# Performance work log

Hardware: AMD Instinct MI355X
Metric: run time of the kernel (lower is better)

Reference implementation:

```python
import jax, jax.numpy as jnp
import numpy as np
import math

B, T, NC = 16, 256, 2
_NS = (9, 9, 11, 11, 9, 20)  # legacy6 region node counts
_OUT, _RF, _FD, _NH, _FF = 32, 64, 128, 4, 2048


def _region_adj(n):
    # chain + second-order edges (legacy6), plus self-loops; GCN sym-normalized
    A = np.zeros((n, n), np.float32)
    for i in range(n - 1):
        A[i, i + 1] = A[i + 1, i] = 1.0
    for i in range(n - 2):
        A[i, i + 2] = A[i + 2, i] = 1.0
    A = A + np.eye(n, dtype=np.float32)
    d = A.sum(1) ** -0.5
    return jnp.asarray(d[:, None] * A * d[None, :])

_ADJS = [_region_adj(n) for n in _NS]


def _pe_table(t, d):
    pos = np.arange(t, dtype=np.float32)[:, None]
    div = np.exp(np.arange(0, d, 2, dtype=np.float32) * (-math.log(10000.0) / d))
    pe = np.zeros((t, d), np.float32)
    pe[:, 0::2] = np.sin(pos * div)
    pe[:, 1::2] = np.cos(pos * div)
    return jnp.asarray(pe)

_PE = _pe_table(T, _FD)


def _ln(x, g, b, eps=1e-5):
    m = jnp.mean(x, -1, keepdims=True)
    v = jnp.mean((x - m) ** 2, -1, keepdims=True)
    return (x - m) / jnp.sqrt(v + eps) * g + b


def _mha(q, kv, qkv_w, qkv_b, ow, ob, nh):
    d = q.shape[-1]
    hd = d // nh
    wq, wk, wv = jnp.split(qkv_w, 3, axis=1)
    bq, bk, bv = jnp.split(qkv_b, 3)
    def sp(x):
        return x.reshape(x.shape[0], x.shape[1], nh, hd).transpose(0, 2, 1, 3)
    Q, K, V = sp(q @ wq + bq), sp(kv @ wk + bk), sp(kv @ wv + bv)
    att = jax.nn.softmax(jnp.einsum('bhqd,bhkd->bhqk', Q, K) / jnp.sqrt(jnp.float32(hd)), axis=-1)
    o = jnp.einsum('bhqk,bhkd->bhqd', att, V).transpose(0, 2, 1, 3).reshape(q.shape[0], q.shape[1], d)
    return o @ ow + ob


def _tel(x, qkv_w, qkv_b, ow, ob, l1g, l1b, f1w, f1b, f2w, f2b, l2g, l2b, nh):
    # torch post-norm TransformerEncoderLayer (relu FFN, eval mode: no dropout)
    x = _ln(x + _mha(x, x, qkv_w, qkv_b, ow, ob, nh), l1g, l1b)
    ff = jax.nn.relu(x @ f1w + f1b) @ f2w + f2b
    return _ln(x + ff, l2g, l2b)


def setup_inputs() -> dict:
    key = jax.random.key(0)
    ks = iter(jax.random.split(key, 80))
    def nrm(shape, s=0.05):
        return jax.random.normal(next(ks), shape, jnp.float32) * s
    inp = {}
    for name, n in zip(('x_ljaw', 'x_rjaw', 'x_leye', 'x_reye', 'x_nose', 'x_mouth'), _NS):
        inp[name] = jax.random.normal(next(ks), (B, T, n, 11), jnp.float32)
    inp['global_feats'] = jax.random.normal(next(ks), (B, T, 4), jnp.float32)
    inp['global_alpha'] = jnp.float32(0.2)
    inp['gcn1_w'] = nrm((6, 11, _OUT)); inp['gcn1_b'] = jnp.zeros((6, _OUT))
    inp['gcn2_w'] = nrm((6, _OUT, _OUT)); inp['gcn2_b'] = jnp.zeros((6, _OUT))
    inp['rln_g'] = jnp.ones((6, _RF)); inp['rln_b'] = jnp.zeros((6, _RF))
    inp['sp_qkv_w'] = nrm((_RF, 3 * _RF)); inp['sp_qkv_b'] = jnp.zeros((3 * _RF,))
    inp['sp_out_w'] = nrm((_RF, _RF)); inp['sp_out_b'] = jnp.zeros((_RF,))
    inp['sp_ln1_g'] = jnp.ones((_RF,)); inp['sp_ln1_b'] = jnp.zeros((_RF,))
    inp['sp_ff1_w'] = nrm((_RF, _FF)); inp['sp_ff1_b'] = jnp.zeros((_FF,))
    inp['sp_ff2_w'] = nrm((_FF, _RF)); inp['sp_ff2_b'] = jnp.zeros((_RF,))
    inp['sp_ln2_g'] = jnp.ones((_RF,)); inp['sp_ln2_b'] = jnp.zeros((_RF,))
    priors = np.array([0.3, 0.3, 0.8, 0.8, 0.4, 1.0], np.float32)
    inp['region_logits'] = jnp.asarray(np.log(np.expm1(priors)).reshape(1, 6, 1))
    inp['gate1_w'] = nrm((_RF, 32)); inp['gate1_b'] = jnp.zeros((32,))
    inp['gate2_w'] = nrm((32, 1)); inp['gate2_b'] = jnp.zeros((1,))
    inp['ca_qkv_w'] = nrm((_RF, 3 * _RF)); inp['ca_qkv_b'] = jnp.zeros((3 * _RF,))
    inp['ca_out_w'] = nrm((_RF, _RF)); inp['ca_out_b'] = jnp.zeros((_RF,))
    inp['ca_ln_g'] = jnp.ones((_RF,)); inp['ca_ln_b'] = jnp.zeros((_RF,))
    inp['glob_w'] = nrm((4, _RF)); inp['glob_b'] = jnp.zeros((_RF,))
    inp['glob_ln_g'] = jnp.ones((_RF,)); inp['glob_ln_b'] = jnp.zeros((_RF,))
    inp['fused_ln_g'] = jnp.ones((_FD,)); inp['fused_ln_b'] = jnp.zeros((_FD,))
    inp['tp_qkv_w'] = nrm((_FD, 3 * _FD)); inp['tp_qkv_b'] = jnp.zeros((3 * _FD,))
    inp['tp_out_w'] = nrm((_FD, _FD)); inp['tp_out_b'] = jnp.zeros((_FD,))
    inp['tp_ln1_g'] = jnp.ones((_FD,)); inp['tp_ln1_b'] = jnp.zeros((_FD,))
    inp['tp_ff1_w'] = nrm((_FD, _FF)); inp['tp_ff1_b'] = jnp.zeros((_FF,))
    inp['tp_ff2_w'] = nrm((_FF, _FD)); inp['tp_ff2_b'] = jnp.zeros((_FD,))
    inp['tp_ln2_g'] = jnp.ones((_FD,)); inp['tp_ln2_b'] = jnp.zeros((_FD,))
    inp['attnproj_w'] = nrm((_FD, 1)); inp['attnproj_b'] = jnp.zeros((1,))
    inp['cls1_w'] = nrm((_FD, _OUT)); inp['cls1_b'] = jnp.zeros((_OUT,))
    inp['cls_ln_g'] = jnp.ones((_OUT,)); inp['cls_ln_b'] = jnp.zeros((_OUT,))
    inp['cls2_w'] = nrm((_OUT, NC)); inp['cls2_b'] = jnp.zeros((NC,))
    return inp


def reference(x_ljaw, x_rjaw, x_leye, x_reye, x_nose, x_mouth, global_feats, global_alpha, gcn1_w, gcn1_b, gcn2_w, gcn2_b, rln_g, rln_b, sp_qkv_w, sp_qkv_b, sp_out_w, sp_out_b, sp_ln1_g, sp_ln1_b, sp_ff1_w, sp_ff1_b, sp_ff2_w, sp_ff2_b, sp_ln2_g, sp_ln2_b, region_logits, gate1_w, gate1_b, gate2_w, gate2_b, ca_qkv_w, ca_qkv_b, ca_out_w, ca_out_b, ca_ln_g, ca_ln_b, glob_w, glob_b, glob_ln_g, glob_ln_b, fused_ln_g, fused_ln_b, tp_qkv_w, tp_qkv_b, tp_out_w, tp_out_b, tp_ln1_g, tp_ln1_b, tp_ff1_w, tp_ff1_b, tp_ff2_w, tp_ff2_b, tp_ln2_g, tp_ln2_b, attnproj_w, attnproj_b, cls1_w, cls1_b, cls_ln_g, cls_ln_b, cls2_w, cls2_b):
    xs = (x_ljaw, x_rjaw, x_leye, x_reye, x_nose, x_mouth)
    Bc, Tc = x_ljaw.shape[0], x_ljaw.shape[1]
    # per-region 2-layer GCN + concat(mean,max) node pooling -> (B,T,64) tokens
    toks = []
    for i in range(6):
        A = _ADJS[i]
        h = jax.nn.relu(jnp.einsum('nm,btmf->btnf', A, xs[i] @ gcn1_w[i]) + gcn1_b[i])
        h = jax.nn.relu(jnp.einsum('nm,btmf->btnf', A, h @ gcn2_w[i]) + gcn2_b[i])
        feat = jnp.concatenate([h.mean(2), h.max(2)], -1)
        toks.append(_ln(feat, rln_g[i], rln_b[i]))
    tok = jnp.stack(toks, 2).reshape(Bc * Tc, 6, _RF)
    # spatial transformer over the 6 region tokens per frame
    tok = _tel(tok, sp_qkv_w, sp_qkv_b, sp_out_w, sp_out_b, sp_ln1_g, sp_ln1_b, sp_ff1_w, sp_ff1_b, sp_ff2_w, sp_ff2_b, sp_ln2_g, sp_ln2_b, _NH)
    # learned region priors (softplus) * per-sample sigmoid gates
    rw = jax.nn.softplus(region_logits)
    gate = jax.nn.sigmoid(jax.nn.relu(tok @ gate1_w + gate1_b) @ gate2_w + gate2_b)
    tok = tok * rw * gate
    # cross-attn fusion: mean-region query attends over region tokens
    q = jnp.mean(tok, 1, keepdims=True)
    attn = _mha(q, tok, ca_qkv_w, ca_qkv_b, ca_out_w, ca_out_b, _NH)
    fused_r = _ln(q[:, 0] + attn[:, 0], ca_ln_g, ca_ln_b)
    # gated global branch (4 -> 64), concat to fused_dim=128
    g = jax.nn.relu(_ln(global_feats.reshape(Bc * Tc, 4) @ glob_w + glob_b, glob_ln_g, glob_ln_b))
    g = jnp.tanh(global_alpha) * g
    fused = _ln(jnp.concatenate([fused_r, g], -1), fused_ln_g, fused_ln_b).reshape(Bc, Tc, _FD)
    # temporal transformer + attention pooling over time
    fused = fused + _PE[None, :Tc]
    h = _tel(fused, tp_qkv_w, tp_qkv_b, tp_out_w, tp_out_b, tp_ln1_g, tp_ln1_b, tp_ff1_w, tp_ff1_b, tp_ff2_w, tp_ff2_b, tp_ln2_g, tp_ln2_b, _NH)
    wt = jax.nn.softmax(h @ attnproj_w + attnproj_b, axis=1)
    pooled = jnp.sum(wt * h, 1)
    z = jax.nn.relu(_ln(pooled @ cls1_w + cls1_b, cls_ln_g, cls_ln_b))
    return z @ cls2_w + cls2_b
```

## Files before the change

kernel.cpp:

```cpp
#include <hip/hip_runtime.h>
#include <math.h>
#include <stddef.h>

#define NFRM 4096
#define NBATCH 16

typedef __attribute__((ext_vector_type(8))) short short8v;
typedef __attribute__((ext_vector_type(4))) float f32x4;
#define MFMA_BF16(a,b,c) __builtin_amdgcn_mfma_f32_16x16x32_bf16(a,b,c,0,0,0)

__device__ inline float wsum64(float v){
  #pragma unroll
  for(int m=32;m>=1;m>>=1) v += __shfl_xor(v, m, 64);
  return v;
}

__device__ inline float pe_val(int t,int d){
  int k = d >> 1;
  float div = expf(-(float)(2*k) * (9.210340371976184f/128.f));
  float ang = (float)t * div;
  return (d & 1) ? cosf(ang) : sinf(ang);
}

__device__ inline void bf16split(float x, unsigned short &h, unsigned short &l){
  unsigned u = __float_as_uint(x);
  unsigned r = (u + 0x7FFFu + ((u>>16)&1u)) & 0xFFFF0000u;
  h = (unsigned short)(r>>16);
  float rem = x - __uint_as_float(r);
  unsigned u2 = __float_as_uint(rem);
  unsigned r2 = (u2 + 0x7FFFu + ((u2>>16)&1u));
  l = (unsigned short)(r2>>16);
}

__global__ __launch_bounds__(64) void pack_all_kernel(
    const float* __restrict__ spf1w, const float* __restrict__ spf2w,
    const float* __restrict__ tpf1w, const float* __restrict__ tpf2w,
    unsigned short* __restrict__ sp1h, unsigned short* __restrict__ sp1l,
    unsigned short* __restrict__ sp2h, unsigned short* __restrict__ sp2l,
    unsigned short* __restrict__ tp1h, unsigned short* __restrict__ tp1l,
    unsigned short* __restrict__ tp2h, unsigned short* __restrict__ tp2l)
{
  int b = blockIdx.x, lane = threadIdx.x;
  const float* w; unsigned short *hi, *lo; int K, N, ntile, s;
  if(b < 256){        w=spf1w; hi=sp1h; lo=sp1l; K=64;   N=2048; ntile=b&127;        s=b>>7; }
  else if(b < 512){   int bb=b-256;  w=spf2w; hi=sp2h; lo=sp2l; K=2048; N=64;   ntile=bb&3;   s=bb>>2; }
  else if(b < 1024){  int bb=b-512;  w=tpf1w; hi=tp1h; lo=tp1l; K=128;  N=2048; ntile=bb&127; s=bb>>7; }
  else {              int bb=b-1024; w=tpf2w; hi=tp2h; lo=tp2l; K=2048; N=128;  ntile=bb&7;   s=bb>>3; }
  int n = ntile*16 + (lane & 15);
  int k0 = s*32 + (lane>>4)*8;
  size_t off = (((size_t)ntile*(K/32) + s)*64 + lane)*8;
  #pragma unroll
  for(int e=0;e<8;e++){
    float v = w[(size_t)(k0+e)*N + n];
    unsigned short h,l;
    bf16split(v,h,l);
    hi[off+e]=h; lo[off+e]=l;
  }
}

template<int D, int NS>
__global__ __launch_bounds__(256) void ffn_mfma_partial(
    const float* __restrict__ X, float* __restrict__ P,
    const unsigned short* __restrict__ w1h, const unsigned short* __restrict__ w1l,
    const float* __restrict__ b1,
    const unsigned short* __restrict__ w2h, const unsigned short* __restrict__ w2l)
{
  constexpr int TM=32, JC=128;
  constexpr int KS1 = D/32;
  constexpr int NT2W = (D/16)/4;
  constexpr int HS = 2048/NS;
  constexpr int NCH = HS/JC;
  constexpr int HP = JC + 8;
  __shared__ unsigned short Hh[TM][HP];
  __shared__ unsigned short Hl[TM][HP];
  int tid = threadIdx.x;
  int lane = tid & 63, w = tid >> 6;
  int ar = lane & 15, ak = lane >> 4;
  size_t Ntok = (size_t)gridDim.x*TM;
  const float* Xb = X + (size_t)blockIdx.x*TM*D;

  short8v xah[2][KS1], xal[2][KS1];
  #pragma unroll
  for(int mt=0;mt<2;mt++){
    #pragma unroll
    for(int s=0;s<KS1;s++){
      const float* xp = Xb + (size_t)(mt*16+ar)*D + s*32 + ak*8;
      #pragma unroll
      for(int e=0;e<8;e++){
        unsigned short h,l;
        bf16split(xp[e],h,l);
        xah[mt][s][e]=(short)h; xal[mt][s][e]=(short)l;
      }
    }
  }

  f32x4 acc2[2][NT2W];
  #pragma unroll
  for(int mt=0;mt<2;mt++)
    #pragma unroll
    for(int nt=0;nt<NT2W;nt++)
      acc2[mt][nt] = (f32x4){0.f,0.f,0.f,0.f};

  for(int ch=0; ch<NCH; ch++){
    int jc = blockIdx.y*HS + ch*JC;
    f32x4 a1[2][2];
    #pragma unroll
    for(int mt=0;mt<2;mt++){ a1[mt][0]=(f32x4){0,0,0,0}; a1[mt][1]=(f32x4){0,0,0,0}; }
    #pragma unroll
    for(int s=0;s<KS1;s++){
      #pragma unroll
      for(int nt=0;nt<2;nt++){
        int ntile1 = (jc + w*32 + nt*16) >> 4;
        size_t off = (((size_t)ntile1*KS1 + s)*64 + lane)*8;
        short8v bh = *(const short8v*)(w1h + off);
        short8v bl = *(const short8v*)(w1l + off);
        #pragma unroll
        for(int mt=0;mt<2;mt++){
          a1[mt][nt] = MFMA_BF16(xah[mt][s], bh, a1[mt][nt]);
          a1[mt][nt] = MFMA_BF16(xah[mt][s], bl, a1[mt][nt]);
          a1[mt][nt] = MFMA_BF16(xal[mt][s], bh, a1[mt][nt]);
        }
      }
    }
    __syncthreads();
    #pragma unroll
    for(int nt=0;nt<2;nt++){
      int colBase = w*32 + nt*16 + ar;
      float bval = b1[jc + colBase];
      #pragma unroll
      for(int mt=0;mt<2;mt++){
        #pragma unroll
        for(int r=0;r<4;r++){
          float hv = a1[mt][nt][r] + bval;
          hv = fmaxf(hv, 0.f);
          unsigned short h,l;
          bf16split(hv,h,l);
          int row = mt*16 + ak*4 + r;
          Hh[row][colBase]=h; Hl[row][colBase]=l;
        }
      }
    }
    __syncthreads();
    #pragma unroll
    for(int s2=0;s2<4;s2++){
      short8v ah[2], al[2];
      #pragma unroll
      for(int mt=0;mt<2;mt++){
        ah[mt] = *(const short8v*)&Hh[mt*16+ar][s2*32 + ak*8];
        al[mt] = *(const short8v*)&Hl[mt*16+ar][s2*32 + ak*8];
      }
      #pragma unroll
      for(int nt=0;nt<NT2W;nt++){
        int ntile2 = w*NT2W + nt;
        int kstep2 = (jc >> 5) + s2;
        size_t off = (((size_t)ntile2*64 + kstep2)*64 + lane)*8;
        short8v bh = *(const short8v*)(w2h + off);
        short8v bl = *(const short8v*)(w2l + off);
        #pragma unroll
        for(int mt=0;mt<2;mt++){
          acc2[mt][nt] = MFMA_BF16(ah[mt], bh, acc2[mt][nt]);
          acc2[mt][nt] = MFMA_BF16(ah[mt], bl, acc2[mt][nt]);
          acc2[mt][nt] = MFMA_BF16(al[mt], bh, acc2[mt][nt]);
        }
      }
    }
  }
  float* Pb = P + (size_t)blockIdx.y*Ntok*D + (size_t)blockIdx.x*TM*D;
  #pragma unroll
  for(int mt=0;mt<2;mt++){
    #pragma unroll
    for(int nt=0;nt<NT2W;nt++){
      int col = (w*NT2W + nt)*16 + ar;
      #pragma unroll
      for(int r=0;r<4;r++){
        int row = mt*16 + ak*4 + r;
        Pb[(size_t)row*D + col] = acc2[mt][nt][r];
      }
    }
  }
}

template<int D, int NS>
__global__ __launch_bounds__(256) void ffn_combine_kernel(
    const float* __restrict__ X, const float* __restrict__ P,
    float* __restrict__ Y,
    const float* __restrict__ b2,
    const float* __restrict__ lg, const float* __restrict__ lb)
{
  constexpr int EPL = D/64;
  int tid=threadIdx.x;
  int lane = tid & 63;
  size_t Ntok = (size_t)gridDim.x*4;
  size_t row = (size_t)blockIdx.x*4 + (tid>>6);
  size_t base = row*D;
  float e[EPL];
  float s=0.f;
  #pragma unroll
  for(int i=0;i<EPL;i++){
    int c = i*64+lane;
    float v = X[base+c] + b2[c];
    #pragma unroll
    for(int sp=0;sp<NS;sp++) v += P[(size_t)sp*Ntok*D + base + c];
    e[i]=v; s+=v;
  }
  float mm = wsum64(s)*(1.f/D);
  float s2=0.f;
  #pragma unroll
  for(int i=0;i<EPL;i++){ float d=e[i]-mm; s2+=d*d; }
  float rs = rsqrtf(wsum64(s2)*(1.f/D)+1e-5f);
  #pragma unroll
  for(int i=0;i<EPL;i++){
    int c=i*64+lane;
    Y[base+c] = (e[i]-mm)*rs*lg[c]+lb[c];
  }
}

__global__ __launch_bounds__(128) void gcn_kernel(
    const float* __restrict__ x0,const float* __restrict__ x1,
    const float* __restrict__ x2,const float* __restrict__ x3,
    const float* __restrict__ x4,const float* __restrict__ x5,
    const float* __restrict__ g1w,const float* __restrict__ g1b,
    const float* __restrict__ g2w,const float* __restrict__ g2b,
    const float* __restrict__ rg,const float* __restrict__ rb,
    float* __restrict__ tok)
{
  int tid=threadIdx.x;
  int lane = tid & 63, w = tid >> 6;
  int f = blockIdx.x*2 + w;
  int r = blockIdx.y;
  int n = (r==5) ? 20 : ((r==2 || r==3) ? 11 : 9);
  const float* xr = (r==0)?x0:(r==1)?x1:(r==2)?x2:(r==3)?x3:(r==4)?x4:x5;
  int c = lane & 31;

  __shared__ float xs[2][20*12];
  __shared__ float t0g[2][24*32];
  __shared__ float t1s[2][20*32];
  __shared__ float Cw[2][20][5];

  float W1c[11], W2c[32];
  #pragma unroll
  for(int k=0;k<11;k++) W1c[k]=g1w[r*352 + k*32 + c];
  #pragma unroll
  for(int k=0;k<32;k++) W2c[k]=g2w[r*1024 + k*32 + c];
  float b1c = g1b[r*32+c], b2c = g2b[r*32+c];

  for(int i=lane;i<100;i+=64){
    int node=i/5, j=i%5, m=node+j-2;
    float cf=0.f;
    if(node<n && m>=0 && m<n){
      int di = 1 + min(node,2) + min(n-1-node,2);
      int dm = 1 + min(m,2) + min(n-1-m,2);
      cf = rsqrtf((float)(di*dm));
    }
    Cw[w][node][j]=cf;
  }
  for(int i=lane;i<128;i+=64){
    int row4=i>>5, col=i&31;
    int row = (row4<2) ? row4 : (n+row4);
    t0g[w][row*32+col]=0.f;
  }
  for(int i=lane;i<n*12;i+=64){
    int node=i/12, k=i-node*12;
    xs[w][i] = (k<11) ? xr[(size_t)f*n*11 + node*11 + k] : 0.f;
  }
  __builtin_amdgcn_wave_barrier();
  for(int i=lane;i<n*32;i+=64){
    int node=i>>5;
    float4 xa = *(const float4*)&xs[w][node*12];
    float4 xb = *(const float4*)&xs[w][node*12+4];
    float4 xc = *(const float4*)&xs[w][node*12+8];
    float s = xa.x*W1c[0]+xa.y*W1c[1]+xa.z*W1c[2]+xa.w*W1c[3]
            + xb.x*W1c[4]+xb.y*W1c[5]+xb.z*W1c[6]+xb.w*W1c[7]
            + xc.x*W1c[8]+xc.y*W1c[9]+xc.z*W1c[10];
    t0g[w][(node+2)*32+c]=s;
  }
  __builtin_amdgcn_wave_barrier();
  for(int i=lane;i<n*32;i+=64){
    int node=i>>5;
    float s=b1c;
    #pragma unroll
    for(int j=0;j<5;j++) s += Cw[w][node][j]*t0g[w][(node+j)*32+c];
    t1s[w][i]=fmaxf(s,0.f);
  }
  __builtin_amdgcn_wave_barrier();
  for(int i=lane;i<n*32;i+=64){
    int node=i>>5;
    float s=0.f;
    #pragma unroll
    for(int k0=0;k0<32;k0+=4){
      float4 tv = *(const float4*)&t1s[w][node*32+k0];
      s += tv.x*W2c[k0] + tv.y*W2c[k0+1] + tv.z*W2c[k0+2] + tv.w*W2c[k0+3];
    }
    t0g[w][(node+2)*32+c]=s;
  }
  __builtin_amdgcn_wave_barrier();
  for(int i=lane;i<n*32;i+=64){
    int node=i>>5;
    float s=b2c;
    #pragma unroll
    for(int j=0;j<5;j++) s += Cw[w][node][j]*t0g[w][(node+j)*32+c];
    t1s[w][i]=fmaxf(s,0.f);
  }
  __builtin_amdgcn_wave_barrier();
  float v;
  if(lane<32){
    float s=0.f;
    for(int m=0;m<n;m++) s += t1s[w][m*32+lane];
    v = s/(float)n;
  } else {
    float mx=-1e30f;
    for(int m=0;m<n;m++) mx = fmaxf(mx, t1s[w][m*32+c]);
    v = mx;
  }
  float m1 = wsum64(v)*(1.f/64.f);
  float d1 = v - m1;
  float var = wsum64(d1*d1)*(1.f/64.f);
  float y = d1*rsqrtf(var+1e-5f)*rg[r*64+lane] + rb[r*64+lane];
  tok[((size_t)f*6+r)*64+lane] = y;
}

__global__ __launch_bounds__(256) void sp_attn_kernel(
    float* __restrict__ tok,
    const float* __restrict__ qkvw,const float* __restrict__ qkvb,
    const float* __restrict__ ow,const float* __restrict__ ob,
    const float* __restrict__ l1g,const float* __restrict__ l1b)
{
  __shared__ float Xs[24][64];
  __shared__ float QKV[24][192];
  __shared__ float SC[4][144];
  __shared__ float AO[24][64];
  int tid=threadIdx.x;
  int f0 = blockIdx.x*4;
  float* Xf = &Xs[0][0];
  for(int i=tid;i<1536;i+=256) Xf[i] = tok[(size_t)f0*384 + i];
  __syncthreads();
  {
    int cg = tid & 31, c0 = cg*6;
    int rg = tid >> 5, r0 = rg*3;
    float acc[3][6];
    #pragma unroll
    for(int m=0;m<3;m++)
      #pragma unroll
      for(int j=0;j<6;j++) acc[m][j]=qkvb[c0+j];
    for(int k=0;k<64;k++){
      float wv[6];
      #pragma unroll
      for(int j=0;j<6;j++) wv[j]=qkvw[k*192+c0+j];
      float xv0=Xs[r0][k], xv1=Xs[r0+1][k], xv2=Xs[r0+2][k];
      #pragma unroll
      for(int j=0;j<6;j++){
        acc[0][j]+=xv0*wv[j];
        acc[1][j]+=xv1*wv[j];
        acc[2][j]+=xv2*wv[j];
      }
    }
    #pragma unroll
    for(int m=0;m<3;m++)
      #pragma unroll
      for(int j=0;j<6;j++) QKV[r0+m][c0+j]=acc[m][j];
  }
  __syncthreads();
  for(int i=tid;i<576;i+=256){
    int fr=i/144, rest=i%144;
    int h=rest/36, qi=(rest%36)/6, ki=rest%6;
    float s=0.f;
    #pragma unroll
    for(int d=0;d<16;d++) s += QKV[fr*6+qi][h*16+d]*QKV[fr*6+ki][64+h*16+d];
    SC[fr][rest]=s*0.25f;
  }
  __syncthreads();
  if(tid<96){
    int fr=tid/24, idx=tid%24;
    int base=idx*6;
    float mx=-1e30f;
    for(int k=0;k<6;k++) mx=fmaxf(mx,SC[fr][base+k]);
    float sm=0.f;
    for(int k=0;k<6;k++){ float e=expf(SC[fr][base+k]-mx); SC[fr][base+k]=e; sm+=e; }
    float rr=1.f/sm;
    for(int k=0;k<6;k++) SC[fr][base+k]*=rr;
  }
  __syncthreads();
  for(int i=tid;i<1536;i+=256){
    int fr=i/384, rem=i%384;
    int row=rem/64, c=rem&63, h=c/16;
    float s=0.f;
    #pragma unroll
    for(int k=0;k<6;k++) s += SC[fr][h*36+row*6+k]*QKV[fr*6+k][128+c];
    AO[fr*6+row][c]=s;
  }
  __syncthreads();
  {
    int cg = tid & 31, c0 = cg*2;
    int rg = tid >> 5, r0 = rg*3;
    float acc[3][2];
    #pragma unroll
    for(int m=0;m<3;m++){ acc[m][0]=ob[c0]; acc[m][1]=ob[c0+1]; }
    for(int k=0;k<64;k++){
      float w0=ow[k*64+c0], w1=ow[k*64+c0+1];
      float a0=AO[r0][k], a1=AO[r0+1][k], a2=AO[r0+2][k];
      acc[0][0]+=a0*w0; acc[0][1]+=a0*w1;
      acc[1][0]+=a1*w0; acc[1][1]+=a1*w1;
      acc[2][0]+=a2*w0; acc[2][1]+=a2*w1;
    }
    #pragma unroll
    for(int m=0;m<3;m++){
      QKV[r0+m][c0]   = Xs[r0+m][c0]   + acc[m][0];
      QKV[r0+m][c0+1] = Xs[r0+m][c0+1] + acc[m][1];
    }
  }
  __syncthreads();
  {
    int lane = tid & 63, w = tid >> 6;
    #pragma unroll
    for(int rr=0;rr<6;rr++){
      int row = w*6+rr;
      float v=QKV[row][lane];
      float mm=wsum64(v)*(1.f/64.f);
      float d=v-mm;
      float var=wsum64(d*d)*(1.f/64.f);
      tok[(size_t)f0*384 + row*64 + lane]=d*rsqrtf(var+1e-5f)*l1g[lane]+l1b[lane];
    }
  }
}

template<int D, int TM>
__global__ __launch_bounds__(256) void ffn_ln_kernel(
    const float* __restrict__ X, float* __restrict__ Yout,
    const float* __restrict__ w1,const float* __restrict__ b1,
    const float* __restrict__ w2,const float* __restrict__ b2,
    const float* __restrict__ lg,const float* __restrict__ lb)
{
  constexpr int JC = 128;
  constexpr int JS = JC + 4;
  constexpr int M1 = TM/8;
  constexpr int CG = D/4;
  constexpr int MG2 = 256/CG;
  constexpr int M2 = TM/MG2;
  __shared__ float Xs[TM*D];
  __shared__ float Hs[TM*JS];
  int tid=threadIdx.x;
  const float* Xb = X + (size_t)blockIdx.x*TM*D;
  for(int i=tid;i<TM*D;i+=256) Xs[i]=Xb[i];

  int jg = tid & 31, j0 = jg*4;
  int mg1 = tid >> 5;
  int m10 = mg1*M1;
  int cg = tid % CG, c0 = cg*4;
  int mg2 = tid / CG;
  int m20 = mg2*M2;

  float acc[M2][4];
  #pragma unroll
  for(int m=0;m<M2;m++){ acc[m][0]=0.f;acc[m][1]=0.f;acc[m][2]=0.f;acc[m][3]=0.f; }

  __syncthreads();
  for(int jc=0;jc<2048;jc+=JC){
    float a1[M1][4];
    float4 bv = *(const float4*)&b1[jc+j0];
    #pragma unroll
    for(int m=0;m<M1;m++){ a1[m][0]=bv.x;a1[m][1]=bv.y;a1[m][2]=bv.z;a1[m][3]=bv.w; }
    for(int k0=0;k0<D;k0+=4){
      float4 wr0 = *(const float4*)&w1[(size_t)(k0+0)*2048 + jc + j0];
      float4 wr1 = *(const float4*)&w1[(size_t)(k0+1)*2048 + jc + j0];
      float4 wr2 = *(const float4*)&w1[(size_t)(k0+2)*2048 + jc + j0];
      float4 wr3 = *(const float4*)&w1[(size_t)(k0+3)*2048 + jc + j0];
      #pragma unroll
      for(int m=0;m<M1;m++){
        float4 xv = *(const float4*)&Xs[(m10+m)*D + k0];
        a1[m][0] += xv.x*wr0.x + xv.y*wr1.x + xv.z*wr2.x + xv.w*wr3.x;
        a1[m][1] += xv.x*wr0.y + xv.y*wr1.y + xv.z*wr2.y + xv.w*wr3.y;
        a1[m][2] += xv.x*wr0.z + xv.y*wr1.z + xv.z*wr2.z + xv.w*wr3.z;
        a1[m][3] += xv.x*wr0.w + xv.y*wr1.w + xv.z*wr2.w + xv.w*wr3.w;
      }
    }
    #pragma unroll
    for(int m=0;m<M1;m++){
      float4 hv;
      hv.x=fmaxf(a1[m][0],0.f); hv.y=fmaxf(a1[m][1],0.f);
      hv.z=fmaxf(a1[m][2],0.f); hv.w=fmaxf(a1[m][3],0.f);
      *(float4*)&Hs[(m10+m)*JS + j0] = hv;
    }
    __syncthreads();
    for(int jj0=0;jj0<JC;jj0+=4){
      float4 w20 = *(const float4*)&w2[(size_t)(jc+jj0+0)*D + c0];
      float4 w21 = *(const float4*)&w2[(size_t)(jc+jj0+1)*D + c0];
      float4 w22 = *(const float4*)&w2[(size_t)(jc+jj0+2)*D + c0];
      float4 w23 = *(const float4*)&w2[(size_t)(jc+jj0+3)*D + c0];
      #pragma unroll
      for(int m=0;m<M2;m++){
        float4 hv = *(const float4*)&Hs[(m20+m)*JS + jj0];
        acc[m][0] += hv.x*w20.x + hv.y*w21.x + hv.z*w22.x + hv.w*w23.x;
        acc[m][1] += hv.x*w20.y + hv.y*w21.y + hv.z*w22.y + hv.w*w23.y;
        acc[m][2] += hv.x*w20.z + hv.y*w21.z + hv.z*w22.z + hv.w*w23.z;
        acc[m][3] += hv.x*w20.w + hv.y*w21.w + hv.z*w22.w + hv.w*w23.w;
      }
    }
    __syncthreads();
  }
  {
    float4 b2v = *(const float4*)&b2[c0];
    #pragma unroll
    for(int m=0;m<M2;m++){
      int row = m20+m;
      float4 xv = *(const float4*)&Xs[row*D + c0];
      float4 yv;
      yv.x = xv.x + acc[m][0] + b2v.x;
      yv.y = xv.y + acc[m][1] + b2v.y;
      yv.z = xv.z + acc[m][2] + b2v.z;
      yv.w = xv.w + acc[m][3] + b2v.w;
      *(float4*)&Hs[row*D + c0] = yv;
    }
  }
  __syncthreads();
  constexpr int EPL = D/64;
  int lane = tid & 63, wv = tid >> 6;
  float* Yb = Yout + (size_t)blockIdx.x*TM*D;
  for(int row=wv; row<TM; row+=4){
    float e[EPL];
    float s=0.f;
    #pragma unroll
    for(int i=0;i<EPL;i++){ e[i]=Hs[row*D + i*64 + lane]; s+=e[i]; }
    float mm = wsum64(s)*(1.f/D);
    float s2=0.f;
    #pragma unroll
    for(int i=0;i<EPL;i++){ float d=e[i]-mm; s2+=d*d; }
    float rs = rsqrtf(wsum64(s2)*(1.f/D)+1e-5f);
    #pragma unroll
    for(int i=0;i<EPL;i++)
      Yb[row*D + i*64 + lane] = (e[i]-mm)*rs*lg[i*64+lane]+lb[i*64+lane];
  }
}

__global__ __launch_bounds__(256) void fuse_kernel(
    const float* __restrict__ tok, const float* __restrict__ gfeat,
    const float* __restrict__ alpha_p, const float* __restrict__ rlogit,
    const float* __restrict__ g1w,const float* __restrict__ g1b,
    const float* __restrict__ g2w,const float* __restrict__ g2b,
    const float* __restrict__ caqw,const float* __restrict__ caqb,
    const float* __restrict__ caow,const float* __restrict__ caob,
    const float* __restrict__ calng,const float* __restrict__ calnb,
    const float* __restrict__ gw,const float* __restrict__ gb,
    const float* __restrict__ glng,const float* __restrict__ glnb,
    const float* __restrict__ flng,const float* __restrict__ flnb,
    float* __restrict__ fused)
{
  int tid=threadIdx.x;
  int lane = tid & 63, w = tid >> 6;
  int f = blockIdx.x*4 + w;
  __shared__ float X[4][384];
  __shared__ float G1[4][192];
  __shared__ float gt[4][6];
  __shared__ float qv[4][64];
  __shared__ float Qs[4][64];
  __shared__ float KK[4][384], VV[4][384];
  __shared__ float sc[4][24];
  __shared__ float AOs[4][64];

  const float* trow = tok + (size_t)f*384;
  for(int i=lane;i<384;i+=64) X[w][i]=trow[i];
  __syncthreads();
  for(int i=lane;i<192;i+=64){
    int rr=i/32, j=i%32;
    float s=g1b[j];
    #pragma unroll
    for(int k=0;k<64;k++) s += X[w][rr*64+k]*g1w[k*32+j];
    G1[w][i]=fmaxf(s,0.f);
  }
  __syncthreads();
  if(lane<6){
    float s=g2b[0];
    #pragma unroll
    for(int k=0;k<32;k++) s += G1[w][lane*32+k]*g2w[k];
    float gate = 1.f/(1.f+expf(-s));
    float rw = log1pf(expf(rlogit[lane]));
    gt[w][lane]=gate*rw;
  }
  __syncthreads();
  for(int i=lane;i<384;i+=64) X[w][i]*=gt[w][i/64];
  __syncthreads();
  {
    float s=0.f;
    #pragma unroll
    for(int rr=0;rr<6;rr++) s+=X[w][rr*64+lane];
    qv[w][lane]=s*(1.f/6.f);
  }
  __syncthreads();
  {
    float s=caqb[lane];
    #pragma unroll
    for(int k=0;k<64;k++) s += qv[w][k]*caqw[k*192+lane];
    Qs[w][lane]=s;
  }
  for(int i=lane;i<384;i+=64){
    int rr=i/64, c=i%64;
    float sk=caqb[64+c], sv=caqb[128+c];
    #pragma unroll
    for(int k=0;k<64;k++){
      float xv=X[w][rr*64+k];
      sk += xv*caqw[k*192+64+c];
      sv += xv*caqw[k*192+128+c];
    }
    KK[w][i]=sk; VV[w][i]=sv;
  }
  __syncthreads();
  if(lane<24){
    int h=lane/6, ki=lane%6;
    float s=0.f;
    #pragma unroll
    for(int d=0;d<16;d++) s += Qs[w][h*16+d]*KK[w][ki*64+h*16+d];
    sc[w][lane]=s*0.25f;
  }
  __syncthreads();
  if(lane<4){
    float mx=-1e30f;
    for(int k=0;k<6;k++) mx=fmaxf(mx,sc[w][lane*6+k]);
    float sm=0.f;
    for(int k=0;k<6;k++){ float e=expf(sc[w][lane*6+k]-mx); sc[w][lane*6+k]=e; sm+=e; }
    float rr=1.f/sm;
    for(int k=0;k<6;k++) sc[w][lane*6+k]*=rr;
  }
  __syncthreads();
  {
    int h=lane/16;
    float s=0.f;
    #pragma unroll
    for(int k=0;k<6;k++) s += sc[w][h*6+k]*VV[w][k*64+lane];
    AOs[w][lane]=s;
  }
  __syncthreads();
  float pr;
  {
    float s=caob[lane];
    #pragma unroll
    for(int k=0;k<64;k++) s += AOs[w][k]*caow[k*64+lane];
    pr = qv[w][lane] + s;
  }
  float m1=wsum64(pr)*(1.f/64.f);
  float d1=pr-m1;
  float v1=wsum64(d1*d1)*(1.f/64.f);
  float fr = d1*rsqrtf(v1+1e-5f)*calng[lane]+calnb[lane];
  float gvv;
  {
    float s=gb[lane];
    #pragma unroll
    for(int k=0;k<4;k++) s += gfeat[(size_t)f*4+k]*gw[k*64+lane];
    gvv=s;
  }
  float m2=wsum64(gvv)*(1.f/64.f);
  float d2=gvv-m2;
  float v2=wsum64(d2*d2)*(1.f/64.f);
  float gg = fmaxf(d2*rsqrtf(v2+1e-5f)*glng[lane]+glnb[lane],0.f)*tanhf(alpha_p[0]);
  float sm_ = wsum64(fr+gg)*(1.f/128.f);
  float da=fr-sm_, db=gg-sm_;
  float vv = wsum64(da*da+db*db)*(1.f/128.f);
  float rs = rsqrtf(vv+1e-5f);
  int t = f & 255;
  fused[(size_t)f*128+lane]     = da*rs*flng[lane]+flnb[lane]         + pe_val(t,lane);
  fused[(size_t)f*128+64+lane]  = db*rs*flng[64+lane]+flnb[64+lane]   + pe_val(t,64+lane);
}

__global__ __launch_bounds__(256) void tqkv_gemm_kernel(
    const float* __restrict__ X, float* __restrict__ Y,
    const float* __restrict__ w, const float* __restrict__ b)
{
  __shared__ float Xs[32*128];
  int tid=threadIdx.x;
  const float* Xb = X + (size_t)blockIdx.x*32*128;
  for(int i=tid;i<4096;i+=256) Xs[i]=Xb[i];
  __syncthreads();
  int cg = tid & 31, c0 = cg*4;
  int mg = tid >> 5, m0 = mg*4;
  float* Yb = Y + (size_t)blockIdx.x*32*384;
  int oc = blockIdx.y*128;
  float acc[4][4];
  float4 bv = *(const float4*)&b[oc+c0];
  #pragma unroll
  for(int m=0;m<4;m++){ acc[m][0]=bv.x;acc[m][1]=bv.y;acc[m][2]=bv.z;acc[m][3]=bv.w; }
  for(int k0=0;k0<128;k0+=4){
    float4 w0 = *(const float4*)&w[(k0+0)*384 + oc + c0];
    float4 w1 = *(const float4*)&w[(k0+1)*384 + oc + c0];
    float4 w2 = *(const float4*)&w[(k0+2)*384 + oc + c0];
    float4 w3 = *(const float4*)&w[(k0+3)*384 + oc + c0];
    #pragma unroll
    for(int m=0;m<4;m++){
      float4 xv = *(const float4*)&Xs[(m0+m)*128 + k0];
      acc[m][0] += xv.x*w0.x + xv.y*w1.x + xv.z*w2.x + xv.w*w3.x;
      acc[m][1] += xv.x*w0.y + xv.y*w1.y + xv.z*w2.y + xv.w*w3.y;
      acc[m][2] += xv.x*w0.z + xv.y*w1.z + xv.z*w2.z + xv.w*w3.z;
      acc[m][3] += xv.x*w0.w + xv.y*w1.w + xv.z*w2.w + xv.w*w3.w;
    }
  }
  #pragma unroll
  for(int m=0;m<4;m++){
    float4 yv; yv.x=acc[m][0];yv.y=acc[m][1];yv.z=acc[m][2];yv.w=acc[m][3];
    *(float4*)&Yb[(m0+m)*384 + oc + c0] = yv;
  }
}

__global__ __launch_bounds__(256) void tattn_split_kernel(
    const float* __restrict__ qkv, float* __restrict__ PO,
    float* __restrict__ PM, float* __restrict__ PL)
{
  int b=blockIdx.x, h=blockIdx.y, s=blockIdx.z, tid=threadIdx.x;
  __shared__ float Ksh[32*32];
  __shared__ float Vsh[32*32];
  const float* base = qkv + (size_t)b*256*384;
  int k0 = s*32;
  for(int i=tid;i<1024;i+=256){
    int t=i>>5, d=i&31;
    Ksh[i]=base[(size_t)(k0+t)*384+128+h*32+d];
    Vsh[i]=base[(size_t)(k0+t)*384+256+h*32+d];
  }
  float q[32];
  #pragma unroll
  for(int d=0;d<32;d++) q[d]=base[(size_t)tid*384+h*32+d];
  __syncthreads();
  const float scale=0.17677669529663687f;
  float sc[32];
  float mx=-1e30f;
  #pragma unroll
  for(int k=0;k<32;k++){
    float sv=0.f;
    #pragma unroll
    for(int d=0;d<32;d++) sv += q[d]*Ksh[k*32+d];
    sc[k]=sv*scale;
    mx=fmaxf(mx,sc[k]);
  }
  float l=0.f, o[32];
  #pragma unroll
  for(int d=0;d<32;d++) o[d]=0.f;
  #pragma unroll
  for(int k=0;k<32;k++){
    float p=expf(sc[k]-mx);
    l+=p;
    #pragma unroll
    for(int d=0;d<32;d++) o[d]+=p*Vsh[k*32+d];
  }
  int bh = b*4+h;
  size_t idx = ((size_t)s*64 + bh)*256 + tid;
  PM[idx]=mx; PL[idx]=l;
  float* po = PO + idx*32;
  #pragma unroll
  for(int d=0;d<32;d++) po[d]=o[d];
}

__global__ __launch_bounds__(256) void attn_combine_kernel(
    const float* __restrict__ PO, const float* __restrict__ PM,
    const float* __restrict__ PL, float* __restrict__ obuf)
{
  int tid=threadIdx.x;
  int ql = tid>>5, d = tid&31;
  int bh = blockIdx.x >> 5;
  int qc = blockIdx.x & 31;
  int q = qc*8 + ql;
  float ms[8], ls[8];
  float M=-1e30f;
  #pragma unroll
  for(int s=0;s<8;s++){
    size_t idx = ((size_t)s*64 + bh)*256 + q;
    ms[s]=PM[idx]; ls[s]=PL[idx];
    M=fmaxf(M,ms[s]);
  }
  float L=0.f, ov=0.f;
  #pragma unroll
  for(int s=0;s<8;s++){
    float w = expf(ms[s]-M);
    L += ls[s]*w;
    size_t idx = ((size_t)s*64 + bh)*256 + q;
    ov += w * PO[idx*32 + d];
  }
  int b = bh>>2, h = bh&3;
  obuf[(size_t)(b*256+q)*128 + h*32 + d] = ov / L;
}

__global__ __launch_bounds__(256) void tattn_kernel(
    const float* __restrict__ qkv, float* __restrict__ obuf)
{
  int b=blockIdx.x, h=blockIdx.y, tid=threadIdx.x;
  __shared__ float Ksh[256*32];
  __shared__ float Vsh[64*32];
  const float* base = qkv + (size_t)b*256*384;
  for(int i=tid;i<8192;i+=256){
    int t=i>>5, d=i&31;
    Ksh[i]=base[t*384+128+h*32+d];
  }
  float q[32];
  #pragma unroll
  for(int d=0;d<32;d++) q[d]=base[(size_t)tid*384+h*32+d];
  __syncthreads();
  const float scale=0.17677669529663687f;
  float mx=-1e30f;
  for(int k=0;k<256;k++){
    float s=0.f;
    #pragma unroll
    for(int d=0;d<32;d++) s += q[d]*Ksh[k*32+d];
    mx=fmaxf(mx,s*scale);
  }
  float l=0.f, o[32];
  #pragma unroll
  for(int d=0;d<32;d++) o[d]=0.f;
  for(int kc=0;kc<256;kc+=64){
    __syncthreads();
    for(int i=tid;i<2048;i+=256){
      int t=i>>5, d=i&31;
      Vsh[i]=base[(size_t)(kc+t)*384+256+h*32+d];
    }
    __syncthreads();
    for(int k2=0;k2<64;k2++){
      float s=0.f;
      #pragma unroll
      for(int d=0;d<32;d++) s += q[d]*Ksh[(kc+k2)*32+d];
      float p=expf(s*scale-mx);
      l+=p;
      #pragma unroll
      for(int d=0;d<32;d++) o[d]+=p*Vsh[k2*32+d];
    }
  }
  float inv=1.f/l;
  float* orow = obuf + (size_t)(b*256+tid)*128 + h*32;
  #pragma unroll
  for(int d=0;d<32;d++) orow[d]=o[d]*inv;
}

__global__ __launch_bounds__(256) void tproj_gemm_kernel(
    const float* __restrict__ O, float* __restrict__ F,
    const float* __restrict__ w, const float* __restrict__ b,
    const float* __restrict__ lg, const float* __restrict__ lb)
{
  __shared__ float Os[32*128];
  __shared__ float Ys[32*128];
  int tid=threadIdx.x;
  const float* Ob = O + (size_t)blockIdx.x*32*128;
  float* Fb = F + (size_t)blockIdx.x*32*128;
  for(int i=tid;i<4096;i+=256) Os[i]=Ob[i];
  __syncthreads();
  int cg = tid & 31, c0 = cg*4;
  int mg = tid >> 5, m0 = mg*4;
  float acc[4][4];
  float4 bv = *(const float4*)&b[c0];
  #pragma unroll
  for(int m=0;m<4;m++){ acc[m][0]=bv.x;acc[m][1]=bv.y;acc[m][2]=bv.z;acc[m][3]=bv.w; }
  for(int k0=0;k0<128;k0+=4){
    float4 w0 = *(const float4*)&w[(k0+0)*128 + c0];
    float4 w1 = *(const float4*)&w[(k0+1)*128 + c0];
    float4 w2 = *(const float4*)&w[(k0+2)*128 + c0];
    float4 w3 = *(const float4*)&w[(k0+3)*128 + c0];
    #pragma unroll
    for(int m=0;m<4;m++){
      float4 xv = *(const float4*)&Os[(m0+m)*128 + k0];
      acc[m][0] += xv.x*w0.x + xv.y*w1.x + xv.z*w2.x + xv.w*w3.x;
      acc[m][1] += xv.x*w0.y + xv.y*w1.y + xv.z*w2.y + xv.w*w3.y;
      acc[m][2] += xv.x*w0.z + xv.y*w1.z + xv.z*w2.z + xv.w*w3.z;
      acc[m][3] += xv.x*w0.w + xv.y*w1.w + xv.z*w2.w + xv.w*w3.w;
    }
  }
  #pragma unroll
  for(int m=0;m<4;m++){
    float4 fv = *(const float4*)&Fb[(m0+m)*128 + c0];
    float4 yv;
    yv.x = fv.x + acc[m][0]; yv.y = fv.y + acc[m][1];
    yv.z = fv.z + acc[m][2]; yv.w = fv.w + acc[m][3];
    *(float4*)&Ys[(m0+m)*128 + c0] = yv;
  }
  __syncthreads();
  int lane = tid & 63, wv = tid >> 6;
  for(int row=wv; row<32; row+=4){
    float e0=Ys[row*128+lane], e1=Ys[row*128+64+lane];
    float mm = wsum64(e0+e1)*(1.f/128.f);
    float d0=e0-mm, d1=e1-mm;
    float rs = rsqrtf(wsum64(d0*d0+d1*d1)*(1.f/128.f)+1e-5f);
    Fb[row*128+lane]    = d0*rs*lg[lane]+lb[lane];
    Fb[row*128+64+lane] = d1*rs*lg[64+lane]+lb[64+lane];
  }
}

__global__ __launch_bounds__(256) void pool_cls_kernel(
    const float* __restrict__ h2,
    const float* __restrict__ apw,const float* __restrict__ apb,
    const float* __restrict__ c1w,const float* __restrict__ c1b,
    const float* __restrict__ clng,const float* __restrict__ clnb,
    const float* __restrict__ c2w,const float* __restrict__ c2b,
    float* __restrict__ out)
{
  int b=blockIdx.x, tid=threadIdx.x;
  __shared__ float lg[256];
  __shared__ float wt[256];
  __shared__ float invs[1];
  __shared__ float pooled[128];
  __shared__ float z[32];
  const float* H = h2 + (size_t)b*256*128;
  {
    float s=apb[0];
    #pragma unroll
    for(int k=0;k<128;k++) s += H[(size_t)tid*128+k]*apw[k];
    lg[tid]=s;
  }
  __syncthreads();
  if(tid==0){
    float mx=-1e30f;
    for(int i=0;i<256;i++) mx=fmaxf(mx,lg[i]);
    float sm=0.f;
    for(int i=0;i<256;i++){ float e=expf(lg[i]-mx); wt[i]=e; sm+=e; }
    invs[0]=1.f/sm;
  }
  __syncthreads();
  float inv=invs[0];
  if(tid<128){
    float s=0.f;
    for(int t=0;t<256;t++) s += wt[t]*inv*H[(size_t)t*128+tid];
    pooled[tid]=s;
  }
  __syncthreads();
  if(tid<32){
    float s=c1b[tid];
    #pragma unroll
    for(int k=0;k<128;k++) s += pooled[k]*c1w[k*32+tid];
    z[tid]=s;
  }
  __syncthreads();
  if(tid==0){
    float m=0.f;
    for(int i=0;i<32;i++) m+=z[i];
    m *= (1.f/32.f);
    float v=0.f;
    for(int i=0;i<32;i++){ float d=z[i]-m; v+=d*d; }
    v *= (1.f/32.f);
    float rs=rsqrtf(v+1e-5f);
    for(int i=0;i<32;i++) z[i]=fmaxf((z[i]-m)*rs*clng[i]+clnb[i],0.f);
  }
  __syncthreads();
  if(tid<2){
    float s=c2b[tid];
    #pragma unroll
    for(int k=0;k<32;k++) s += z[k]*c2w[k*2+tid];
    out[b*2+tid]=s;
  }
}

extern "C" void kernel_launch(void* const* d_in, const int* in_sizes, int n_in,
                              void* d_out, int out_size, void* d_ws, size_t ws_size,
                              hipStream_t stream) {
  const float* x0 = (const float*)d_in[0];
  const float* x1 = (const float*)d_in[1];
  const float* x2 = (const float*)d_in[2];
  const float* x3 = (const float*)d_in[3];
  const float* x4 = (const float*)d_in[4];
  const float* x5 = (const float*)d_in[5];
  const float* gfeat   = (const float*)d_in[6];
  const float* alpha_p = (const float*)d_in[7];
  const float* g1w = (const float*)d_in[8];
  const float* g1b = (const float*)d_in[9];
  const float* g2w = (const float*)d_in[10];
  const float* g2b = (const float*)d_in[11];
  const float* rlg = (const float*)d_in[12];
  const float* rlb = (const float*)d_in[13];
  const float* spqkvw = (const float*)d_in[14];
  const float* spqkvb = (const float*)d_in[15];
  const float* spow = (const float*)d_in[16];
  const float* spob = (const float*)d_in[17];
  const float* spl1g = (const float*)d_in[18];
  const float* spl1b = (const float*)d_in[19];
  const float* spf1w = (const float*)d_in[20];
  const float* spf1b = (const float*)d_in[21];
  const float* spf2w = (const float*)d_in[22];
  const float* spf2b = (const float*)d_in[23];
  const float* spl2g = (const float*)d_in[24];
  const float* spl2b = (const float*)d_in[25];
  const float* rlogit = (const float*)d_in[26];
  const float* gate1w = (const float*)d_in[27];
  const float* gate1b = (const float*)d_in[28];
  const float* gate2w = (const float*)d_in[29];
  const float* gate2b = (const float*)d_in[30];
  const float* caqkvw = (const float*)d_in[31];
  const float* caqkvb = (const float*)d_in[32];
  const float* caow = (const float*)d_in[33];
  const float* caob = (const float*)d_in[34];
  const float* calng = (const float*)d_in[35];
  const float* calnb = (const float*)d_in[36];
  const float* globw = (const float*)d_in[37];
  const float* globb = (const float*)d_in[38];
  const float* glng = (const float*)d_in[39];
  const float* glnb = (const float*)d_in[40];
  const float* flng = (const float*)d_in[41];
  const float* flnb = (const float*)d_in[42];
  const float* tpqkvw = (const float*)d_in[43];
  const float* tpqkvb = (const float*)d_in[44];
  const float* tpow = (const float*)d_in[45];
  const float* tpob = (const float*)d_in[46];
  const float* tpl1g = (const float*)d_in[47];
  const float* tpl1b = (const float*)d_in[48];
  const float* tpf1w = (const float*)d_in[49];
  const float* tpf1b = (const float*)d_in[50];
  const float* tpf2w = (const float*)d_in[51];
  const float* tpf2b = (const float*)d_in[52];
  const float* tpl2g = (const float*)d_in[53];
  const float* tpl2b = (const float*)d_in[54];
  const float* apw = (const float*)d_in[55];
  const float* apb = (const float*)d_in[56];
  const float* c1w = (const float*)d_in[57];
  const float* c1b = (const float*)d_in[58];
  const float* clng = (const float*)d_in[59];
  const float* clnb = (const float*)d_in[60];
  const float* c2w = (const float*)d_in[61];
  const float* c2b = (const float*)d_in[62];

  float* ws = (float*)d_ws;
  float* tok   = ws;
  float* fused = tok   + (size_t)NFRM*384;
  float* qkv   = fused + (size_t)NFRM*128;
  float* obuf  = qkv   + (size_t)NFRM*384;
  float* part  = obuf  + (size_t)NFRM*128;
  size_t part_elems = (size_t)2*24576*64;
  unsigned short* pk = (unsigned short*)(part + part_elems);
  unsigned short* sp1h = pk;
  unsigned short* sp1l = sp1h + 131072;
  unsigned short* sp2h = sp1l + 131072;
  unsigned short* sp2l = sp2h + 131072;
  unsigned short* tp1h = sp2l + 131072;
  unsigned short* tp1l = tp1h + 262144;
  unsigned short* tp2h = tp1l + 262144;
  unsigned short* tp2l = tp2h + 262144;
  size_t pack_ushorts = 4*131072 + 4*262144;
  size_t need = ((size_t)NFRM*384 + NFRM*128 + NFRM*384 + NFRM*128 + part_elems)*4
              + pack_ushorts*2;
  bool mfma_ok = (ws_size >= need);

  float* attnPO = (float*)(pk + pack_ushorts);
  float* attnPM = attnPO + (size_t)8*64*256*32;
  float* attnPL = attnPM + (size_t)8*64*256;
  size_t need2 = need + ((size_t)8*64*256*32 + 2*(size_t)8*64*256)*4;
  bool attn_ok = (ws_size >= need2);

  if(mfma_ok){
    pack_all_kernel<<<1536,64,0,stream>>>(spf1w,spf2w,tpf1w,tpf2w,
                                          sp1h,sp1l,sp2h,sp2l,tp1h,tp1l,tp2h,tp2l);
  }

  gcn_kernel<<<dim3(NFRM/2,6),128,0,stream>>>(x0,x1,x2,x3,x4,x5,g1w,g1b,g2w,g2b,rlg,rlb,tok);
  sp_attn_kernel<<<NFRM/4,256,0,stream>>>(tok,spqkvw,spqkvb,spow,spob,spl1g,spl1b);
  if(mfma_ok){
    ffn_mfma_partial<64,2><<<dim3(768,2),256,0,stream>>>(tok,part,sp1h,sp1l,spf1b,sp2h,sp2l);
    ffn_combine_kernel<64,2><<<24576/4,256,0,stream>>>(tok,part,tok,spf2b,spl2g,spl2b);
  } else {
    ffn_ln_kernel<64,32><<<768,256,0,stream>>>(tok,tok,spf1w,spf1b,spf2w,spf2b,spl2g,spl2b);
  }
  fuse_kernel<<<NFRM/4,256,0,stream>>>(tok,gfeat,alpha_p,rlogit,gate1w,gate1b,gate2w,gate2b,
                                    caqkvw,caqkvb,caow,caob,calng,calnb,
                                    globw,globb,glng,glnb,flng,flnb,fused);
  tqkv_gemm_kernel<<<dim3(128,3),256,0,stream>>>(fused,qkv,tpqkvw,tpqkvb);
  if(attn_ok){
    tattn_split_kernel<<<dim3(NBATCH,4,8),256,0,stream>>>(qkv,attnPO,attnPM,attnPL);
    attn_combine_kernel<<<64*32,256,0,stream>>>(attnPO,attnPM,attnPL,obuf);
  } else {
    tattn_kernel<<<dim3(NBATCH,4),256,0,stream>>>(qkv,obuf);
  }
  tproj_gemm_kernel<<<128,256,0,stream>>>(obuf,fused,tpow,tpob,tpl1g,tpl1b);
  if(mfma_ok){
    ffn_mfma_partial<128,4><<<dim3(128,4),256,0,stream>>>(fused,part,tp1h,tp1l,tpf1b,tp2h,tp2l);
    ffn_combine_kernel<128,4><<<NFRM/4,256,0,stream>>>(fused,part,obuf,tpf2b,tpl2g,tpl2b);
  } else {
    ffn_ln_kernel<128,16><<<256,256,0,stream>>>(fused,obuf,tpf1w,tpf1b,tpf2w,tpf2b,tpl2g,tpl2b);
  }
  pool_cls_kernel<<<NBATCH,256,0,stream>>>(obuf,apw,apb,c1w,c1b,clng,clnb,c2w,c2b,(float*)d_out);
}
```

Before: 333.4 us.

## Register-resident templated GCN and fuse spatial FFN combine into fuse kernel

The GCN kernel is rewritten as a template on node count. Per-node activations stay in registers, and the banded adjacency is applied as degree-scaled sums instead of shared-memory coefficient tables, with four frames per block instead of two. Separately, the spatial FFN's split-K combine, bias add and LayerNorm move into the start of fuse_kernel, which drops one launch and one round trip of the token tensor through global memory. The cost is higher register pressure in the GCN, and the LayerNorm work is redone inside fuse_kernel's wave layout.

```diff
diff --git a/kernel.cpp b/kernel.cpp
--- a/kernel.cpp
+++ b/kernel.cpp
@@ -215,7 +215,90 @@
   }
 }
 
-__global__ __launch_bounds__(128) void gcn_kernel(
+template<int N>
+__device__ inline void gcn_impl(
+    int f, int r, const float* __restrict__ xr,
+    const float* __restrict__ g1w,const float* __restrict__ g1b,
+    const float* __restrict__ g2w,const float* __restrict__ g2b,
+    const float* __restrict__ rg,const float* __restrict__ rb,
+    float* __restrict__ tok, float* xsw, float* t1w, int lane)
+{
+  int c = lane & 31;
+  float W1c[11], W2c[32];
+  #pragma unroll
+  for(int k=0;k<11;k++) W1c[k]=g1w[r*352 + k*32 + c];
+  #pragma unroll
+  for(int k=0;k<32;k++) W2c[k]=g2w[r*1024 + k*32 + c];
+  float b1c = g1b[r*32+c], b2c = g2b[r*32+c];
+
+  for(int i=lane;i<N*12;i+=64){
+    int node=i/12, k=i-node*12;
+    xsw[i] = (k<11) ? xr[(size_t)f*N*11 + node*11 + k] : 0.f;
+  }
+  __builtin_amdgcn_wave_barrier();
+
+  float t0[N];
+  #pragma unroll
+  for(int node=0;node<N;node++){
+    float4 xa = *(const float4*)&xsw[node*12];
+    float4 xb = *(const float4*)&xsw[node*12+4];
+    float4 xc = *(const float4*)&xsw[node*12+8];
+    t0[node] = xa.x*W1c[0]+xa.y*W1c[1]+xa.z*W1c[2]+xa.w*W1c[3]
+             + xb.x*W1c[4]+xb.y*W1c[5]+xb.z*W1c[6]+xb.w*W1c[7]
+             + xc.x*W1c[8]+xc.y*W1c[9]+xc.z*W1c[10];
+  }
+  float u[N+4];
+  u[0]=0.f; u[1]=0.f; u[N+2]=0.f; u[N+3]=0.f;
+  #pragma unroll
+  for(int node=0;node<N;node++){
+    float dv = rsqrtf((float)(1 + (node<2?node:2) + ((N-1-node)<2?(N-1-node):2)));
+    u[node+2] = dv*t0[node];
+  }
+  float t1v[N];
+  #pragma unroll
+  for(int node=0;node<N;node++){
+    float dv = rsqrtf((float)(1 + (node<2?node:2) + ((N-1-node)<2?(N-1-node):2)));
+    float s = u[node]+u[node+1]+u[node+2]+u[node+3]+u[node+4];
+    t1v[node] = fmaxf(dv*s + b1c, 0.f);
+  }
+  if(lane<32){
+    #pragma unroll
+    for(int node=0;node<N;node++) t1w[node*32+c]=t1v[node];
+  }
+  __builtin_amdgcn_wave_barrier();
+  #pragma unroll
+  for(int node=0;node<N;node++){
+    float s=0.f;
+    #pragma unroll
+    for(int k0=0;k0<32;k0+=4){
+      float4 tv = *(const float4*)&t1w[node*32+k0];
+      s += tv.x*W2c[k0] + tv.y*W2c[k0+1] + tv.z*W2c[k0+2] + tv.w*W2c[k0+3];
+    }
+    t0[node]=s;
+  }
+  #pragma unroll
+  for(int node=0;node<N;node++){
+    float dv = rsqrtf((float)(1 + (node<2?node:2) + ((N-1-node)<2?(N-1-node):2)));
+    u[node+2] = dv*t0[node];
+  }
+  float mean=0.f, mx=-1e30f;
+  #pragma unroll
+  for(int node=0;node<N;node++){
+    float dv = rsqrtf((float)(1 + (node<2?node:2) + ((N-1-node)<2?(N-1-node):2)));
+    float s = u[node]+u[node+1]+u[node+2]+u[node+3]+u[node+4];
+    float t3 = fmaxf(dv*s + b2c, 0.f);
+    mean += t3;
+    mx = fmaxf(mx, t3);
+  }
+  float v = (lane<32) ? mean*(1.f/(float)N) : mx;
+  float m1 = wsum64(v)*(1.f/64.f);
+  float d1 = v - m1;
+  float var = wsum64(d1*d1)*(1.f/64.f);
+  float y = d1*rsqrtf(var+1e-5f)*rg[r*64+lane] + rb[r*64+lane];
+  tok[((size_t)f*6+r)*64+lane] = y;
+}
+
+__global__ __launch_bounds__(256) void gcn_kernel(
     const float* __restrict__ x0,const float* __restrict__ x1,
     const float* __restrict__ x2,const float* __restrict__ x3,
     const float* __restrict__ x4,const float* __restrict__ x5,
@@ -226,97 +309,18 @@
 {
   int tid=threadIdx.x;
   int lane = tid & 63, w = tid >> 6;
-  int f = blockIdx.x*2 + w;
+  int f = blockIdx.x*4 + w;
   int r = blockIdx.y;
-  int n = (r==5) ? 20 : ((r==2 || r==3) ? 11 : 9);
-  const float* xr = (r==0)?x0:(r==1)?x1:(r==2)?x2:(r==3)?x3:(r==4)?x4:x5;
-  int c = lane & 31;
-
-  __shared__ float xs[2][20*12];
-  __shared__ float t0g[2][24*32];
-  __shared__ float t1s[2][20*32];
-  __shared__ float Cw[2][20][5];
-
-  float W1c[11], W2c[32];
-  #pragma unroll
-  for(int k=0;k<11;k++) W1c[k]=g1w[r*352 + k*32 + c];
-  #pragma unroll
-  for(int k=0;k<32;k++) W2c[k]=g2w[r*1024 + k*32 + c];
-  float b1c = g1b[r*32+c], b2c = g2b[r*32+c];
-
-  for(int i=lane;i<100;i+=64){
-    int node=i/5, j=i%5, m=node+j-2;
-    float cf=0.f;
-    if(node<n && m>=0 && m<n){
-      int di = 1 + min(node,2) + min(n-1-node,2);
-      int dm = 1 + min(m,2) + min(n-1-m,2);
-      cf = rsqrtf((float)(di*dm));
-    }
-    Cw[w][node][j]=cf;
-  }
-  for(int i=lane;i<128;i+=64){
-    int row4=i>>5, col=i&31;
-    int row = (row4<2) ? row4 : (n+row4);
-    t0g[w][row*32+col]=0.f;
-  }
-  for(int i=lane;i<n*12;i+=64){
-    int node=i/12, k=i-node*12;
-    xs[w][i] = (k<11) ? xr[(size_t)f*n*11 + node*11 + k] : 0.f;
-  }
-  __builtin_amdgcn_wave_barrier();
-  for(int i=lane;i<n*32;i+=64){
-    int node=i>>5;
-    float4 xa = *(const float4*)&xs[w][node*12];
-    float4 xb = *(const float4*)&xs[w][node*12+4];
-    float4 xc = *(const float4*)&xs[w][node*12+8];
-    float s = xa.x*W1c[0]+xa.y*W1c[1]+xa.z*W1c[2]+xa.w*W1c[3]
-            + xb.x*W1c[4]+xb.y*W1c[5]+xb.z*W1c[6]+xb.w*W1c[7]
-            + xc.x*W1c[8]+xc.y*W1c[9]+xc.z*W1c[10];
-    t0g[w][(node+2)*32+c]=s;
-  }
-  __builtin_amdgcn_wave_barrier();
-  for(int i=lane;i<n*32;i+=64){
-    int node=i>>5;
-    float s=b1c;
-    #pragma unroll
-    for(int j=0;j<5;j++) s += Cw[w][node][j]*t0g[w][(node+j)*32+c];
-    t1s[w][i]=fmaxf(s,0.f);
-  }
-  __builtin_amdgcn_wave_barrier();
-  for(int i=lane;i<n*32;i+=64){
-    int node=i>>5;
-    float s=0.f;
-    #pragma unroll
-    for(int k0=0;k0<32;k0+=4){
-      float4 tv = *(const float4*)&t1s[w][node*32+k0];
-      s += tv.x*W2c[k0] + tv.y*W2c[k0+1] + tv.z*W2c[k0+2] + tv.w*W2c[k0+3];
-    }
-    t0g[w][(node+2)*32+c]=s;
-  }
-  __builtin_amdgcn_wave_barrier();
-  for(int i=lane;i<n*32;i+=64){
-    int node=i>>5;
-    float s=b2c;
-    #pragma unroll
-    for(int j=0;j<5;j++) s += Cw[w][node][j]*t0g[w][(node+j)*32+c];
-    t1s[w][i]=fmaxf(s,0.f);
-  }
-  __builtin_amdgcn_wave_barrier();
-  float v;
-  if(lane<32){
-    float s=0.f;
-    for(int m=0;m<n;m++) s += t1s[w][m*32+lane];
-    v = s/(float)n;
-  } else {
-    float mx=-1e30f;
-    for(int m=0;m<n;m++) mx = fmaxf(mx, t1s[w][m*32+c]);
-    v = mx;
-  }
-  float m1 = wsum64(v)*(1.f/64.f);
-  float d1 = v - m1;
-  float var = wsum64(d1*d1)*(1.f/64.f);
-  float y = d1*rsqrtf(var+1e-5f)*rg[r*64+lane] + rb[r*64+lane];
-  tok[((size_t)f*6+r)*64+lane] = y;
+  __shared__ float xs[4][240];
+  __shared__ float t1sh[4][640];
+  float* xsw = &xs[w][0];
+  float* t1w = &t1sh[w][0];
+  if(r==5)             gcn_impl<20>(f,r,x5,g1w,g1b,g2w,g2b,rg,rb,tok,xsw,t1w,lane);
+  else if(r==2)        gcn_impl<11>(f,r,x2,g1w,g1b,g2w,g2b,rg,rb,tok,xsw,t1w,lane);
+  else if(r==3)        gcn_impl<11>(f,r,x3,g1w,g1b,g2w,g2b,rg,rb,tok,xsw,t1w,lane);
+  else if(r==0)        gcn_impl<9>(f,r,x0,g1w,g1b,g2w,g2b,rg,rb,tok,xsw,t1w,lane);
+  else if(r==1)        gcn_impl<9>(f,r,x1,g1w,g1b,g2w,g2b,rg,rb,tok,xsw,t1w,lane);
+  else                 gcn_impl<9>(f,r,x4,g1w,g1b,g2w,g2b,rg,rb,tok,xsw,t1w,lane);
 }
 
 __global__ __launch_bounds__(256) void sp_attn_kernel(
@@ -532,7 +536,9 @@
 }
 
 __global__ __launch_bounds__(256) void fuse_kernel(
-    const float* __restrict__ tok, const float* __restrict__ gfeat,
+    const float* __restrict__ tok, const float* __restrict__ part, int do_combine,
+    const float* __restrict__ sb2, const float* __restrict__ sl2g, const float* __restrict__ sl2b,
+    const float* __restrict__ gfeat,
     const float* __restrict__ alpha_p, const float* __restrict__ rlogit,
     const float* __restrict__ g1w,const float* __restrict__ g1b,
     const float* __restrict__ g2w,const float* __restrict__ g2b,
@@ -557,7 +563,21 @@
   __shared__ float AOs[4][64];
 
   const float* trow = tok + (size_t)f*384;
-  for(int i=lane;i<384;i+=64) X[w][i]=trow[i];
+  if(do_combine){
+    #pragma unroll
+    for(int row=0;row<6;row++){
+      size_t grow = (size_t)f*6 + row;
+      float v = trow[row*64+lane] + sb2[lane]
+              + part[grow*64 + lane]
+              + part[(size_t)24576*64 + grow*64 + lane];
+      float mm = wsum64(v)*(1.f/64.f);
+      float d = v-mm;
+      float var = wsum64(d*d)*(1.f/64.f);
+      X[w][row*64+lane] = d*rsqrtf(var+1e-5f)*sl2g[lane]+sl2b[lane];
+    }
+  } else {
+    for(int i=lane;i<384;i+=64) X[w][i]=trow[i];
+  }
   __syncthreads();
   for(int i=lane;i<192;i+=64){
     int rr=i/32, j=i%32;
@@ -1036,17 +1056,21 @@
                                           sp1h,sp1l,sp2h,sp2l,tp1h,tp1l,tp2h,tp2l);
   }
 
-  gcn_kernel<<<dim3(NFRM/2,6),128,0,stream>>>(x0,x1,x2,x3,x4,x5,g1w,g1b,g2w,g2b,rlg,rlb,tok);
+  gcn_kernel<<<dim3(NFRM/4,6),256,0,stream>>>(x0,x1,x2,x3,x4,x5,g1w,g1b,g2w,g2b,rlg,rlb,tok);
   sp_attn_kernel<<<NFRM/4,256,0,stream>>>(tok,spqkvw,spqkvb,spow,spob,spl1g,spl1b);
   if(mfma_ok){
     ffn_mfma_partial<64,2><<<dim3(768,2),256,0,stream>>>(tok,part,sp1h,sp1l,spf1b,sp2h,sp2l);
-    ffn_combine_kernel<64,2><<<24576/4,256,0,stream>>>(tok,part,tok,spf2b,spl2g,spl2b);
+    fuse_kernel<<<NFRM/4,256,0,stream>>>(tok,part,1,spf2b,spl2g,spl2b,
+                                      gfeat,alpha_p,rlogit,gate1w,gate1b,gate2w,gate2b,
+                                      caqkvw,caqkvb,caow,caob,calng,calnb,
+                                      globw,globb,glng,glnb,flng,flnb,fused);
   } else {
     ffn_ln_kernel<64,32><<<768,256,0,stream>>>(tok,tok,spf1w,spf1b,spf2w,spf2b,spl2g,spl2b);
-  }
-  fuse_kernel<<<NFRM/4,256,0,stream>>>(tok,gfeat,alpha_p,rlogit,gate1w,gate1b,gate2w,gate2b,
-                                    caqkvw,caqkvb,caow,caob,calng,calnb,
-                                    globw,globb,glng,glnb,flng,flnb,fused);
+    fuse_kernel<<<NFRM/4,256,0,stream>>>(tok,part,0,spf2b,spl2g,spl2b,
+                                      gfeat,alpha_p,rlogit,gate1w,gate1b,gate2w,gate2b,
+                                      caqkvw,caqkvb,caow,caob,calng,calnb,
+                                      globw,globb,glng,glnb,flng,flnb,fused);
+  }
   tqkv_gemm_kernel<<<dim3(128,3),256,0,stream>>>(fused,qkv,tpqkvw,tpqkvb);
   if(attn_ok){
     tattn_split_kernel<<<dim3(NBATCH,4,8),256,0,stream>>>(qkv,attnPO,attnPM,attnPL);
```

After: 359.5 us. 7.8% more time.
